# Kernel tuning notes

Measured on AMD Instinct MI355X. Metric: run time of the kernel, lower is better.

## Reference

```python
import jax, jax.numpy as jnp
import numpy as np

DIM = 256
FEATURE_SCALE = 4
NMS_THRESHOLD = 8.0
PRE_NMS_TOPK = 2048
MAX_OUTPUT = 256
MIN_SCORE = 0.2


def conv3d_same(x, w, b):
    # x: [D,H,W,Cin], w: [3,3,3,Cin,Cout] -> [D,H,W,Cout], SAME padding (flax default)
    y = jax.lax.conv_general_dilated(
        x[None], w, window_strides=(1, 1, 1), padding="SAME",
        dimension_numbers=("NDHWC", "DHWIO", "NDHWC"))
    return y[0] + b


def setup_inputs() -> dict:
    key = jax.random.key(0)
    ks = jax.random.split(key, 8)
    D, H, W, C = 16, 64, 64, 256
    feature = jax.random.normal(ks[0], (D, H, W, C), jnp.float32)
    mask = jax.random.bernoulli(ks[1], 0.8, (D * FEATURE_SCALE, H * FEATURE_SCALE, W * FEATURE_SCALE))
    s3a = 1.0 / np.sqrt(27 * C)
    s3b = 1.0 / np.sqrt(27 * DIM)
    s1 = 1.0 / np.sqrt(DIM)
    w0 = jax.random.normal(ks[2], (3, 3, 3, C, DIM), jnp.float32) * s3a
    b0 = jnp.zeros((DIM,), jnp.float32)
    w1 = jax.random.normal(ks[3], (3, 3, 3, DIM, DIM), jnp.float32) * s3b
    b1 = jnp.zeros((DIM,), jnp.float32)
    w_logit = jax.random.normal(ks[4], (DIM, 1), jnp.float32) * s1
    b_logit = jnp.zeros((1,), jnp.float32)
    w_reg = jax.random.normal(ks[5], (DIM, 3), jnp.float32) * s1
    b_reg = jnp.zeros((3,), jnp.float32)
    return dict(feature=feature, mask=mask, w0=w0, b0=b0, w1=w1, b1=b1,
                w_logit=w_logit, b_logit=b_logit, w_reg=w_reg, b_reg=b_reg)


def reference(feature, mask, w0, b0, w1, b1, w_logit, b_logit, w_reg, b_reg):
    # ---- feature mixing: n_layers=2 of conv3d + gelu (flax gelu is approximate/tanh) ----
    x = jax.nn.gelu(conv3d_same(feature, w0, b0))
    x = jax.nn.gelu(conv3d_same(x, w1, b1))
    D, H, W = x.shape[:3]

    # ---- detection block: 1x1 convs are pointwise dense layers ----
    logits = (x @ w_logit + b_logit)[..., 0].reshape(-1)          # [N]
    regressions = (x @ w_reg + b_reg)                              # [D,H,W,3]
    ref_locs = (jnp.moveaxis(jnp.mgrid[:D, :H, :W], 0, -1) + 0.5) * FEATURE_SCALE
    pred_locs = (ref_locs + regressions * FEATURE_SCALE).reshape(-1, 3)  # [N,3]

    # ---- generate_predictions: sigmoid scores, pre-NMS top-k, greedy distance NMS ----
    scores = jax.nn.sigmoid(logits)
    top_scores, idx = jax.lax.top_k(scores, PRE_NMS_TOPK)          # sorted desc
    top_locs = pred_locs[idx]                                      # [K,3]
    d2 = ((top_locs[:, None, :] - top_locs[None, :, :]) ** 2).sum(-1)  # [K,K]
    th2 = NMS_THRESHOLD * NMS_THRESHOLD

    def step(suppressed, i):
        keep_i = (~suppressed[i]) & (top_scores[i] >= MIN_SCORE)
        suppressed = suppressed | (keep_i & (d2[i] < th2))
        return suppressed, keep_i

    _, keep = jax.lax.scan(step, jnp.zeros((PRE_NMS_TOPK,), bool), jnp.arange(PRE_NMS_TOPK))
    sel_scores = jnp.where(keep, top_scores, 0.0)
    out_scores, oidx = jax.lax.top_k(sel_scores, MAX_OUTPUT)       # [M]
    out_locs = top_locs[oidx]                                      # [M,3]

    # ---- mask gather: floor/clip/index, zero out-of-mask scores ----
    pli = jnp.floor(out_locs).astype(jnp.int32)
    bound = jnp.array(mask.shape, jnp.int32) - 1
    plc = jnp.clip(pli, 0, bound)
    in_range = (pli == plc).all(axis=1)
    masked = jnp.where(in_range, mask[plc[:, 0], plc[:, 1], plc[:, 2]], False)
    out_scores = jnp.where(masked, out_scores, 0.0)

    return jnp.concatenate([out_locs, out_scores[:, None]], axis=-1)  # [M,4] = (z,y,x,score)
```

## Files before the change

kernel.cpp:

```cpp
#include <hip/hip_runtime.h>
#include <math.h>

#define Dz 16
#define Hy 64
#define Wx 64
#define CHN 256
#define NVOX (Dz*Hy*Wx)
#define TOPK 2048
#define MAXOUT 256
#define CAND_CAP 4096
#define NBCAP 16
#define NHIST 65536

typedef __attribute__((ext_vector_type(8))) _Float16 h8;
typedef __attribute__((ext_vector_type(8))) unsigned short u16x8;
typedef __attribute__((ext_vector_type(4))) float f32x4;

__device__ __forceinline__ float gelu_tanh(float x) {
    return 0.5f*x*(1.0f + tanhf(0.7978845608028654f*(x + 0.044715f*x*x*x)));
}
__device__ __forceinline__ unsigned f2sort(float f) {
    unsigned u = __float_as_uint(f);
    return (u & 0x80000000u) ? ~u : (u | 0x80000000u);
}
__device__ __forceinline__ float sort2f(unsigned s) {
    unsigned u = (s & 0x80000000u) ? (s & 0x7fffffffu) : ~s;
    return __uint_as_float(u);
}

#define MFMA(d, a, b) d = __builtin_amdgcn_mfma_f32_16x16x32_f16(a, b, d, 0, 0, 0)

__global__ __launch_bounds__(256) void prep_kernel(const float* __restrict__ w0,
        const float* __restrict__ w1, u16x8* __restrict__ wpk0,
        u16x8* __restrict__ wpk1, unsigned* __restrict__ hist,
        unsigned* __restrict__ counter) {
    int b = blockIdx.x, t = threadIdx.x;
    if (b < 1728) {
        int id = b*256 + t;
        int l = (id >= 221184) ? 1 : 0;
        int r = id - l*221184;
        int lane = r & 63, ng = (r >> 6) & 15, kbg = (r >> 10) & 7, tp = r >> 13;
        const float* w = l ? w1 : w0;
        u16x8* dst = l ? wpk1 : wpk0;
        h8 hv, lv;
        #pragma unroll
        for (int j = 0; j < 8; ++j) {
            int k = kbg*32 + (lane >> 4)*8 + j;
            int co = ng*16 + (lane & 15);
            float v = w[((size_t)tp*CHN + k)*CHN + co];
            _Float16 h = (_Float16)v;
            hv[j] = h;
            lv[j] = (_Float16)(v - (float)h);
        }
        size_t base = (((size_t)(tp*8 + kbg)*16 + ng)*2)*64 + lane;
        dst[base]      = __builtin_bit_cast(u16x8, hv);
        dst[base + 64] = __builtin_bit_cast(u16x8, lv);
    } else {
        int zb = b - 1728;
        int i = zb*256 + t;
        hist[i] = 0u; hist[i + 16384] = 0u; hist[i + 32768] = 0u; hist[i + 49152] = 0u;
        if (zb == 0 && t == 0) counter[0] = 0u;
    }
}

template<int LAYER>
__global__ __launch_bounds__(512, 4) void conv_kernel(
        const float* __restrict__ fsrc,
        const unsigned short* __restrict__ hhi, const unsigned short* __restrict__ hlo,
        const u16x8* __restrict__ wpk, const float* __restrict__ bias,
        unsigned short* __restrict__ ohi, unsigned short* __restrict__ olo,
        const float* __restrict__ wlog, const float* __restrict__ blog,
        const float* __restrict__ wreg, const float* __restrict__ breg,
        float* __restrict__ locs, unsigned long long* __restrict__ keys,
        unsigned* __restrict__ hist) {
    __shared__ h8 sm[4224];
    const int tid = threadIdx.x;
    const int lane = tid & 63, w = tid >> 6;
    const int yo = w >> 2, wn = w & 3;
    const int lr = lane & 15, lg = lane >> 4;
    const int z = blockIdx.y, y0 = blockIdx.x*2;

    f32x4 acc[4][4];
    #pragma unroll
    for (int m = 0; m < 4; ++m)
        #pragma unroll
        for (int n = 0; n < 4; ++n) acc[m][n] = (f32x4){0.f,0.f,0.f,0.f};

    for (int dz = 0; dz < 3; ++dz) {
        const int zz = z + dz - 1;
        for (int kc = 0; kc < 4; ++kc) {
            __syncthreads();
            if (LAYER == 0) {
                for (int cidx = tid; cidx < 2112; cidx += 512) {
                    int cd = cidx & 7;
                    int rr = cidx >> 3;
                    int r = rr % 66, iy = rr / 66;
                    int ygl = y0 - 1 + iy, xin = r - 1;
                    h8 hv = {0,0,0,0,0,0,0,0}, lv = {0,0,0,0,0,0,0,0};
                    if (((unsigned)zz < (unsigned)Dz) & ((unsigned)ygl < (unsigned)Hy)
                        & ((unsigned)xin < (unsigned)Wx)) {
                        const float* s = fsrc + ((size_t)((zz*Hy + ygl)*Wx + xin))*CHN
                                              + kc*64 + cd*8;
                        float4 t0 = *(const float4*)s;
                        float4 t1 = *(const float4*)(s + 4);
                        float vv[8] = {t0.x,t0.y,t0.z,t0.w,t1.x,t1.y,t1.z,t1.w};
                        #pragma unroll
                        for (int j = 0; j < 8; ++j) {
                            _Float16 h = (_Float16)vv[j];
                            hv[j] = h;
                            lv[j] = (_Float16)(vv[j] - (float)h);
                        }
                    }
                    int sl = cd ^ (r & 7);
                    sm[(iy*66 + r)*8 + sl] = hv;
                    sm[2112 + (iy*66 + r)*8 + sl] = lv;
                }
            } else {
                for (int cidx = tid; cidx < 4224; cidx += 512) {
                    int c = cidx & 7;
                    int rr = cidx >> 3;
                    int r = rr % 66, tt = rr / 66;
                    int p = tt >> 2, iy = tt & 3;
                    int ygl = y0 - 1 + iy, xin = r - 1;
                    u16x8 v = {0,0,0,0,0,0,0,0};
                    if (((unsigned)zz < (unsigned)Dz) & ((unsigned)ygl < (unsigned)Hy)
                        & ((unsigned)xin < (unsigned)Wx)) {
                        const unsigned short* bp = p ? hlo : hhi;
                        v = *(const u16x8*)(bp + ((size_t)((zz*Hy + ygl)*Wx + xin))*CHN
                                               + kc*64 + (size_t)((c ^ (r & 7)))*8);
                    }
                    sm[cidx] = __builtin_bit_cast(h8, v);
                }
            }
            __syncthreads();
            for (int dy = 0; dy < 3; ++dy) {
                const int iyA = yo + dy;
                const h8* As = sm + iyA*528;
                #pragma unroll
                for (int dx = 0; dx < 3; ++dx) {
                    const int tap = (dz*3 + dy)*3 + dx;
                    #pragma unroll
                    for (int kb = 0; kb < 2; ++kb) {
                        const int kbg = kc*2 + kb;
                        const u16x8* wb = wpk + ((size_t)(tap*8 + kbg)*32 + wn*8)*64 + lane;
                        h8 ah[4], al[4];
                        #pragma unroll
                        for (int m = 0; m < 4; ++m) {
                            const int r = m*16 + lr + dx;
                            const int sl = (kb*4 + lg) ^ (r & 7);
                            ah[m] = As[r*8 + sl];
                            al[m] = As[2112 + r*8 + sl];
                        }
                        #pragma unroll
                        for (int n = 0; n < 4; ++n) {
                            h8 bh = __builtin_bit_cast(h8, wb[(size_t)n*128]);
                            h8 bl = __builtin_bit_cast(h8, wb[(size_t)n*128 + 64]);
                            #pragma unroll
                            for (int m = 0; m < 4; ++m) MFMA(acc[m][n], ah[m], bh);
                            #pragma unroll
                            for (int m = 0; m < 4; ++m) MFMA(acc[m][n], al[m], bh);
                            #pragma unroll
                            for (int m = 0; m < 4; ++m) MFMA(acc[m][n], ah[m], bl);
                        }
                    }
                }
            }
        }
    }

    float bn[4];
    #pragma unroll
    for (int n = 0; n < 4; ++n) bn[n] = bias[wn*64 + n*16 + lr];

    if (LAYER == 0) {
        const int ygl = y0 + yo;
        #pragma unroll
        for (int m = 0; m < 4; ++m) {
            #pragma unroll
            for (int rg = 0; rg < 4; ++rg) {
                const int x = m*16 + lg*4 + rg;
                const size_t vbase = ((size_t)((z*Hy + ygl)*Wx + x))*CHN;
                #pragma unroll
                for (int n = 0; n < 4; ++n) {
                    const int co = wn*64 + n*16 + lr;
                    float g = gelu_tanh(acc[m][n][rg] + bn[n]);
                    _Float16 h = (_Float16)g;
                    _Float16 l = (_Float16)(g - (float)h);
                    ohi[vbase + co] = __builtin_bit_cast(unsigned short, h);
                    olo[vbase + co] = __builtin_bit_cast(unsigned short, l);
                }
            }
        }
    } else {
        float wl[4], wr0[4], wr1[4], wr2[4];
        #pragma unroll
        for (int n = 0; n < 4; ++n) {
            const int co = wn*64 + n*16 + lr;
            wl[n] = wlog[co];
            wr0[n] = wreg[co*3 + 0]; wr1[n] = wreg[co*3 + 1]; wr2[n] = wreg[co*3 + 2];
        }
        float p[4][16];
        #pragma unroll
        for (int c = 0; c < 4; ++c)
            #pragma unroll
            for (int xi = 0; xi < 16; ++xi) p[c][xi] = 0.f;
        #pragma unroll
        for (int m = 0; m < 4; ++m)
            #pragma unroll
            for (int rg = 0; rg < 4; ++rg) {
                const int xi = m*4 + rg;
                #pragma unroll
                for (int n = 0; n < 4; ++n) {
                    float g = gelu_tanh(acc[m][n][rg] + bn[n]);
                    p[0][xi] += g*wl[n];
                    p[1][xi] += g*wr0[n];
                    p[2][xi] += g*wr1[n];
                    p[3][xi] += g*wr2[n];
                }
            }
        #pragma unroll
        for (int st = 0; st < 4; ++st) {
            const int s = 1 << st;
            #pragma unroll
            for (int c = 0; c < 4; ++c)
                #pragma unroll
                for (int xi = 0; xi < 16; ++xi)
                    p[c][xi] += __shfl_xor(p[c][xi], s, 64);
        }
        __syncthreads();
        float* det = (float*)sm;
        if (lr == 0) {
            #pragma unroll
            for (int m = 0; m < 4; ++m)
                #pragma unroll
                for (int rg = 0; rg < 4; ++rg) {
                    const int x = m*16 + lg*4 + rg;
                    #pragma unroll
                    for (int c = 0; c < 4; ++c)
                        det[((yo*64 + x)*4 + c)*4 + wn] = p[c][m*4 + rg];
                }
        }
        __syncthreads();
        {
            const int yo2 = tid >> 8, x = (tid >> 2) & 63, chn = tid & 3;
            const float* dp = det + ((yo2*64 + x)*4 + chn)*4;
            float s = dp[0] + dp[1] + dp[2] + dp[3];
            const int ygl = y0 + yo2;
            const int vg = (z*Hy + ygl)*Wx + x;
            if (chn == 0) {
                float logit = s + blog[0];
                float score = 1.f/(1.f + expf(-logit));
                unsigned sb = f2sort(score);
                keys[vg] = ((unsigned long long)sb << 32)
                         | (unsigned long long)(0xFFFFFFFFu - (unsigned)vg);
                atomicAdd(&hist[sb >> 16], 1u);
            } else {
                float coord = (chn == 1) ? (float)z : (chn == 2) ? (float)ygl : (float)x;
                float loc = (coord + 0.5f)*4.0f + (s + breg[chn-1])*4.0f;
                locs[(size_t)vg*3 + (chn-1)] = loc;
            }
        }
    }
}

__global__ __launch_bounds__(1024) void find_cut_kernel(const unsigned* __restrict__ hist,
                                                        unsigned* __restrict__ cutp) {
    __shared__ unsigned ps[1024];
    __shared__ unsigned fs[64];
    __shared__ int sh_cb;
    __shared__ unsigned sh_acc;
    int t = threadIdx.x;
    unsigned s = 0;
    const unsigned* hp = hist + (size_t)t*64;
    for (int j = 0; j < 64; ++j) s += hp[j];
    ps[t] = s;
    __syncthreads();
    for (int off = 1; off < 1024; off <<= 1) {
        unsigned v = ps[t] + ((t + off < 1024) ? ps[t + off] : 0u);
        __syncthreads();
        ps[t] = v;
        __syncthreads();
    }
    if (ps[t] >= TOPK && (t == 1023 || ps[t+1] < TOPK)) {
        sh_cb = t; sh_acc = (t == 1023) ? 0u : ps[t+1];
    }
    __syncthreads();
    int cb = sh_cb; unsigned acc = sh_acc;
    if (t < 64) {
        unsigned f = acc;
        for (int u = t; u < 64; ++u) f += hist[(size_t)cb*64 + u];
        fs[t] = f;
    }
    __syncthreads();
    if (t < 64) {
        if (fs[t] >= TOPK && (t == 63 || fs[t+1] < TOPK))
            cutp[0] = ((unsigned)(cb*64 + t)) << 16;
    }
}

__global__ void compact_kernel(const unsigned long long* __restrict__ keys,
                               const unsigned* __restrict__ cutp,
                               unsigned* __restrict__ counter,
                               unsigned long long* __restrict__ cand) {
    int i = blockIdx.x*blockDim.x + threadIdx.x;
    unsigned thr = cutp[0];
    unsigned long long k = keys[i];
    if ((unsigned)(k >> 32) >= thr) {
        unsigned p = atomicAdd(counter, 1u);
        if (p < CAND_CAP) cand[p] = k;
    }
}

__global__ __launch_bounds__(128) void rank_kernel(const unsigned* __restrict__ counter,
        const unsigned long long* __restrict__ cand, const float* __restrict__ locs,
        float4* __restrict__ loc4G) {
    __shared__ unsigned long long kbuf[CAND_CAP];
    int t = threadIdx.x;
    int g = blockIdx.x*128 + t;
    int M = (int)*counter; if (M > CAND_CAP) M = CAND_CAP;
    for (int i = t; i < CAND_CAP; i += 128) kbuf[i] = (i < M) ? cand[i] : 0ull;
    __syncthreads();
    if (g >= M) return;
    unsigned long long mykey = kbuf[g];
    int rank = 0;
    for (int j = 0; j < M; ++j) rank += (kbuf[j] > mykey) ? 1 : 0;
    if (rank < TOPK) {
        unsigned idx = 0xFFFFFFFFu - (unsigned)(mykey & 0xFFFFFFFFull);
        float4 v;
        v.x = locs[(size_t)idx*3 + 0];
        v.y = locs[(size_t)idx*3 + 1];
        v.z = locs[(size_t)idx*3 + 2];
        v.w = sort2f((unsigned)(mykey >> 32));
        loc4G[rank] = v;
    }
}

__global__ __launch_bounds__(64) void nbr_kernel(const float4* __restrict__ loc4G,
        unsigned short* __restrict__ nbidx, unsigned char* __restrict__ nbcnt) {
    __shared__ float4 b4[TOPK];
    int t = threadIdx.x;
    int g = blockIdx.x*64 + t;
    for (int i = t; i < TOPK; i += 64) b4[i] = loc4G[i];
    __syncthreads();
    float4 me = b4[g];
    int cnt = 0;
    for (int j = 0; j < TOPK; ++j) {
        float4 o = b4[j];
        float dz = o.x - me.x, dy = o.y - me.y, dx = o.z - me.z;
        float d2 = dz*dz + dy*dy + dx*dx;
        if (d2 < 64.0f && j != g) {
            if (cnt < NBCAP) nbidx[(size_t)g*NBCAP + cnt] = (unsigned short)j;
            cnt++;
        }
    }
    nbcnt[g] = (unsigned char)min(cnt, 255);
}

__global__ __launch_bounds__(512) void nms_kernel(const float4* __restrict__ loc4G,
        const unsigned short* __restrict__ nbidx, const unsigned char* __restrict__ nbcnt,
        const int* __restrict__ mask, float* __restrict__ out) {
    __shared__ float4 p4[TOPK];
    __shared__ unsigned short snb[TOPK*NBCAP];
    __shared__ unsigned char scnt[TOPK];
    __shared__ unsigned char supf[TOPK];
    __shared__ unsigned char keepB[TOPK];
    __shared__ unsigned keepw[64];
    __shared__ int wpre[64];
    __shared__ int sh_nk;
    int t = threadIdx.x;
    for (int i = t; i < TOPK; i += 512) {
        p4[i] = loc4G[i]; scnt[i] = nbcnt[i]; supf[i] = 0; keepB[i] = 0;
    }
    for (int i = t; i < TOPK*NBCAP/8; i += 512)
        ((uint4*)snb)[i] = ((const uint4*)nbidx)[i];
    __syncthreads();
    if (t < 64) {
        const int l = t;
        float cz[32], cy[32], cx[32];
        #pragma unroll
        for (int j = 0; j < 32; ++j) {
            float4 v = p4[l*32 + j];
            cz[j] = v.x; cy[j] = v.y; cx[j] = v.z;
        }
        int myok = 0;
        #pragma unroll
        for (int j = 0; j < 32; ++j) myok += (p4[l*32 + j].w >= 0.2f) ? 1 : 0;
        #pragma unroll
        for (int s = 1; s < 64; s <<= 1) myok += __shfl_xor(myok, s, 64);
        const int NS = myok;
        int keeps = 0;
        for (int i = 0; i < NS; ++i) {
            bool kept = (supf[i] == 0);
            if (kept) {
                if (l == 0) keepB[i] = 1;
                ++keeps;
                const int cnt = scnt[i];
                if (cnt <= NBCAP) {
                    if (l < cnt) supf[snb[i*NBCAP + l]] = 1;
                } else {
                    float4 pv = p4[i];
                    #pragma unroll
                    for (int j = 0; j < 32; ++j) {
                        float dz = cz[j]-pv.x, dy = cy[j]-pv.y, dx = cx[j]-pv.z;
                        if (dz*dz + dy*dy + dx*dx < 64.0f) supf[l*32 + j] = 1;
                    }
                }
                asm volatile("s_waitcnt lgkmcnt(0)" ::: "memory");
                if (keeps >= MAXOUT) break;
            }
        }
    }
    __syncthreads();
    if (t < 64) {
        unsigned wmask = 0u;
        for (int j = 0; j < 32; ++j) wmask |= (keepB[t*32 + j] ? 1u : 0u) << j;
        keepw[t] = wmask;
    }
    __syncthreads();
    if (t < 64) {
        int p = 0;
        for (int j = 0; j < t; ++j) p += __popc(keepw[j]);
        wpre[t] = p;
        if (t == 63) sh_nk = p + __popc(keepw[63]);
    }
    __syncthreads();
    const int nk = sh_nk;
    for (int i = t; i < TOPK; i += 512) {
        unsigned w = keepw[i >> 5];
        bool kp = (w >> (i & 31)) & 1u;
        int rk = wpre[i >> 5] + __popc(w & ((1u << (i & 31)) - 1u));
        int slot = kp ? rk : (nk + (i - rk));
        if (slot < MAXOUT) {
            float4 v = p4[i];
            float lz = v.x, ly = v.y, lx = v.z;
            float sc = kp ? v.w : 0.f;
            int iz = (int)floorf(lz), iy = (int)floorf(ly), ix = (int)floorf(lx);
            int cz2 = min(max(iz,0),Dz*4-1), cy2 = min(max(iy,0),Hy*4-1), cx2 = min(max(ix,0),Wx*4-1);
            bool inr = (iz==cz2) && (iy==cy2) && (ix==cx2);
            float osc = (inr && mask[((size_t)cz2*(Hy*4) + cy2)*(Wx*4) + cx2] != 0) ? sc : 0.f;
            out[slot*4+0] = lz; out[slot*4+1] = ly; out[slot*4+2] = lx; out[slot*4+3] = osc;
        }
    }
}

extern "C" void kernel_launch(void* const* d_in, const int* in_sizes, int n_in,
                              void* d_out, int out_size, void* d_ws, size_t ws_size,
                              hipStream_t stream) {
    const float* feature = (const float*)d_in[0];
    const int*   mask    = (const int*)d_in[1];
    const float* w0   = (const float*)d_in[2];
    const float* b0   = (const float*)d_in[3];
    const float* w1   = (const float*)d_in[4];
    const float* b1   = (const float*)d_in[5];
    const float* wlog = (const float*)d_in[6];
    const float* blog = (const float*)d_in[7];
    const float* wreg = (const float*)d_in[8];
    const float* breg = (const float*)d_in[9];

    char* ws = (char*)d_ws;
    size_t off = 0;
    unsigned short* h1hi = (unsigned short*)(ws + off); off += (size_t)NVOX*CHN*2;
    unsigned short* h1lo = (unsigned short*)(ws + off); off += (size_t)NVOX*CHN*2;
    u16x8* wpk0 = (u16x8*)(ws + off);               off += (size_t)442368*16;
    u16x8* wpk1 = (u16x8*)(ws + off);               off += (size_t)442368*16;
    unsigned long long* keys = (unsigned long long*)(ws + off); off += (size_t)NVOX*8;
    float* locs = (float*)(ws + off);               off += (size_t)NVOX*3*4;
    unsigned* hist = (unsigned*)(ws + off);         off += (size_t)NHIST*4;
    unsigned* counter = (unsigned*)(ws + off);      off += 256;
    unsigned* cutp = counter + 1;
    unsigned long long* cand = (unsigned long long*)(ws + off); off += (size_t)CAND_CAP*8;
    float4* loc4G = (float4*)(ws + off);            off += (size_t)TOPK*16;
    unsigned short* nbidx = (unsigned short*)(ws + off); off += (size_t)TOPK*NBCAP*2;
    unsigned char* nbcnt = (unsigned char*)(ws + off);   off += (size_t)TOPK;
    if (ws_size < off) return;

    prep_kernel<<<1792, 256, 0, stream>>>(w0, w1, wpk0, wpk1, hist, counter);
    dim3 cgrid(Hy/2, Dz);
    conv_kernel<0><<<cgrid, 512, 0, stream>>>(feature, nullptr, nullptr, wpk0, b0,
                                              h1hi, h1lo,
                                              nullptr, nullptr, nullptr, nullptr,
                                              nullptr, nullptr, nullptr);
    conv_kernel<1><<<cgrid, 512, 0, stream>>>(nullptr, h1hi, h1lo, wpk1, b1,
                                              nullptr, nullptr,
                                              wlog, blog, wreg, breg,
                                              locs, keys, hist);
    find_cut_kernel<<<1, 1024, 0, stream>>>(hist, cutp);
    compact_kernel<<<NVOX/256, 256, 0, stream>>>(keys, cutp, counter, cand);
    rank_kernel<<<CAND_CAP/128, 128, 0, stream>>>(counter, cand, locs, loc4G);
    nbr_kernel<<<TOPK/64, 64, 0, stream>>>(loc4G, nbidx, nbcnt);
    nms_kernel<<<1, 512, 0, stream>>>(loc4G, nbidx, nbcnt, mask, (float*)d_out);
}
```

Measured before the change: 1.592 ms.

## Re-tile conv waves to 8x2 MFMA tiles and swizzle block order

Changes each wave's tile in the conv kernels from 4 rows x 64 output channels (one y row) to 8 rows x 32 channels (both y rows), so each wave loads half as many weight fragments from global memory but reads more LDS A fragments. The A fragments are now loaded inside the MFMA loop rather than held in arrays, which may lower register pressure. The grid becomes 1D with a swizzled block-to-(z,y) mapping, likely to improve L2 locality of weight and input reads across concurrently running blocks. The detection-head reduction is restructured to reduce per m-tile and sum 8 wave partials through LDS.

```diff
diff --git a/kernel.cpp b/kernel.cpp
--- a/kernel.cpp
+++ b/kernel.cpp
@@ -75,16 +75,17 @@
         unsigned* __restrict__ hist) {
     __shared__ h8 sm[4224];
     const int tid = threadIdx.x;
-    const int lane = tid & 63, w = tid >> 6;
-    const int yo = w >> 2, wn = w & 3;
+    const int lane = tid & 63, wn = tid >> 6;
     const int lr = lane & 15, lg = lane >> 4;
-    const int z = blockIdx.y, y0 = blockIdx.x*2;
-
-    f32x4 acc[4][4];
+    const int bid = blockIdx.x;
+    const int swz = (bid & 7)*64 + (bid >> 3);
+    const int z = swz >> 5, y0 = (swz & 31)*2;
+
+    f32x4 acc[8][2];
     #pragma unroll
-    for (int m = 0; m < 4; ++m)
-        #pragma unroll
-        for (int n = 0; n < 4; ++n) acc[m][n] = (f32x4){0.f,0.f,0.f,0.f};
+    for (int m = 0; m < 8; ++m)
+        #pragma unroll
+        for (int n = 0; n < 2; ++n) acc[m][n] = (f32x4){0.f,0.f,0.f,0.f};
 
     for (int dz = 0; dz < 3; ++dz) {
         const int zz = z + dz - 1;
@@ -134,33 +135,38 @@
             }
             __syncthreads();
             for (int dy = 0; dy < 3; ++dy) {
-                const int iyA = yo + dy;
-                const h8* As = sm + iyA*528;
                 #pragma unroll
                 for (int dx = 0; dx < 3; ++dx) {
                     const int tap = (dz*3 + dy)*3 + dx;
                     #pragma unroll
                     for (int kb = 0; kb < 2; ++kb) {
                         const int kbg = kc*2 + kb;
-                        const u16x8* wb = wpk + ((size_t)(tap*8 + kbg)*32 + wn*8)*64 + lane;
-                        h8 ah[4], al[4];
+                        const u16x8* wb = wpk + ((size_t)(tap*8 + kbg)*32 + wn*4)*64 + lane;
+                        h8 bh0 = __builtin_bit_cast(h8, wb[0]);
+                        h8 bh1 = __builtin_bit_cast(h8, wb[128]);
                         #pragma unroll
-                        for (int m = 0; m < 4; ++m) {
-                            const int r = m*16 + lr + dx;
+                        for (int m = 0; m < 8; ++m) {
+                            const int iyA = (m >> 2) + dy;
+                            const int r = (m & 3)*16 + lr + dx;
                             const int sl = (kb*4 + lg) ^ (r & 7);
-                            ah[m] = As[r*8 + sl];
-                            al[m] = As[2112 + r*8 + sl];
+                            const int base = (iyA*66 + r)*8 + sl;
+                            h8 ah = sm[base];
+                            h8 al = sm[2112 + base];
+                            MFMA(acc[m][0], ah, bh0);
+                            MFMA(acc[m][0], al, bh0);
+                            MFMA(acc[m][1], ah, bh1);
+                            MFMA(acc[m][1], al, bh1);
                         }
+                        h8 bl0 = __builtin_bit_cast(h8, wb[64]);
+                        h8 bl1 = __builtin_bit_cast(h8, wb[192]);
                         #pragma unroll
-                        for (int n = 0; n < 4; ++n) {
-                            h8 bh = __builtin_bit_cast(h8, wb[(size_t)n*128]);
-                            h8 bl = __builtin_bit_cast(h8, wb[(size_t)n*128 + 64]);
-                            #pragma unroll
-                            for (int m = 0; m < 4; ++m) MFMA(acc[m][n], ah[m], bh);
-                            #pragma unroll
-                            for (int m = 0; m < 4; ++m) MFMA(acc[m][n], al[m], bh);
-                            #pragma unroll
-                            for (int m = 0; m < 4; ++m) MFMA(acc[m][n], ah[m], bl);
+                        for (int m = 0; m < 8; ++m) {
+                            const int iyA = (m >> 2) + dy;
+                            const int r = (m & 3)*16 + lr + dx;
+                            const int sl = (kb*4 + lg) ^ (r & 7);
+                            h8 ah = sm[(iyA*66 + r)*8 + sl];
+                            MFMA(acc[m][0], ah, bl0);
+                            MFMA(acc[m][1], ah, bl1);
                         }
                     }
                 }
@@ -168,21 +174,21 @@
         }
     }
 
-    float bn[4];
+    float bn[2];
     #pragma unroll
-    for (int n = 0; n < 4; ++n) bn[n] = bias[wn*64 + n*16 + lr];
+    for (int n = 0; n < 2; ++n) bn[n] = bias[wn*32 + n*16 + lr];
 
     if (LAYER == 0) {
-        const int ygl = y0 + yo;
-        #pragma unroll
-        for (int m = 0; m < 4; ++m) {
+        #pragma unroll
+        for (int m = 0; m < 8; ++m) {
+            const int ygl = y0 + (m >> 2);
             #pragma unroll
             for (int rg = 0; rg < 4; ++rg) {
-                const int x = m*16 + lg*4 + rg;
+                const int x = (m & 3)*16 + lg*4 + rg;
                 const size_t vbase = ((size_t)((z*Hy + ygl)*Wx + x))*CHN;
                 #pragma unroll
-                for (int n = 0; n < 4; ++n) {
-                    const int co = wn*64 + n*16 + lr;
+                for (int n = 0; n < 2; ++n) {
+                    const int co = wn*32 + n*16 + lr;
                     float g = gelu_tanh(acc[m][n][rg] + bn[n]);
                     _Float16 h = (_Float16)g;
                     _Float16 l = (_Float16)(g - (float)h);
@@ -192,60 +198,58 @@
             }
         }
     } else {
-        float wl[4], wr0[4], wr1[4], wr2[4];
-        #pragma unroll
-        for (int n = 0; n < 4; ++n) {
-            const int co = wn*64 + n*16 + lr;
+        float wl[2], wr0[2], wr1[2], wr2[2];
+        #pragma unroll
+        for (int n = 0; n < 2; ++n) {
+            const int co = wn*32 + n*16 + lr;
             wl[n] = wlog[co];
             wr0[n] = wreg[co*3 + 0]; wr1[n] = wreg[co*3 + 1]; wr2[n] = wreg[co*3 + 2];
         }
-        float p[4][16];
-        #pragma unroll
-        for (int c = 0; c < 4; ++c)
-            #pragma unroll
-            for (int xi = 0; xi < 16; ++xi) p[c][xi] = 0.f;
-        #pragma unroll
-        for (int m = 0; m < 4; ++m)
-            #pragma unroll
-            for (int rg = 0; rg < 4; ++rg) {
-                const int xi = m*4 + rg;
-                #pragma unroll
-                for (int n = 0; n < 4; ++n) {
-                    float g = gelu_tanh(acc[m][n][rg] + bn[n]);
-                    p[0][xi] += g*wl[n];
-                    p[1][xi] += g*wr0[n];
-                    p[2][xi] += g*wr1[n];
-                    p[3][xi] += g*wr2[n];
-                }
-            }
-        #pragma unroll
-        for (int st = 0; st < 4; ++st) {
-            const int s = 1 << st;
+        __syncthreads();
+        float* det = (float*)sm;
+        #pragma unroll
+        for (int m = 0; m < 8; ++m) {
+            float p[4][4];
             #pragma unroll
             for (int c = 0; c < 4; ++c)
                 #pragma unroll
-                for (int xi = 0; xi < 16; ++xi)
-                    p[c][xi] += __shfl_xor(p[c][xi], s, 64);
-        }
-        __syncthreads();
-        float* det = (float*)sm;
-        if (lr == 0) {
+                for (int rg = 0; rg < 4; ++rg) p[c][rg] = 0.f;
             #pragma unroll
-            for (int m = 0; m < 4; ++m)
+            for (int rg = 0; rg < 4; ++rg)
+                #pragma unroll
+                for (int n = 0; n < 2; ++n) {
+                    float g = gelu_tanh(acc[m][n][rg] + bn[n]);
+                    p[0][rg] += g*wl[n];
+                    p[1][rg] += g*wr0[n];
+                    p[2][rg] += g*wr1[n];
+                    p[3][rg] += g*wr2[n];
+                }
+            #pragma unroll
+            for (int st = 0; st < 4; ++st) {
+                const int s = 1 << st;
+                #pragma unroll
+                for (int c = 0; c < 4; ++c)
+                    #pragma unroll
+                    for (int rg = 0; rg < 4; ++rg)
+                        p[c][rg] += __shfl_xor(p[c][rg], s, 64);
+            }
+            if (lr == 0) {
+                const int yrow = m >> 2;
                 #pragma unroll
                 for (int rg = 0; rg < 4; ++rg) {
-                    const int x = m*16 + lg*4 + rg;
+                    const int x = (m & 3)*16 + lg*4 + rg;
                     #pragma unroll
                     for (int c = 0; c < 4; ++c)
-                        det[((yo*64 + x)*4 + c)*4 + wn] = p[c][m*4 + rg];
-                }
+                        det[((yrow*64 + x)*4 + c)*8 + wn] = p[c][rg];
+                }
+            }
         }
         __syncthreads();
         {
-            const int yo2 = tid >> 8, x = (tid >> 2) & 63, chn = tid & 3;
-            const float* dp = det + ((yo2*64 + x)*4 + chn)*4;
-            float s = dp[0] + dp[1] + dp[2] + dp[3];
-            const int ygl = y0 + yo2;
+            const int vox = tid >> 2, chn = tid & 3;
+            const float* dp = det + ((size_t)(vox*4 + chn))*8;
+            float s = dp[0] + dp[1] + dp[2] + dp[3] + dp[4] + dp[5] + dp[6] + dp[7];
+            const int ygl = y0 + (vox >> 6), x = vox & 63;
             const int vg = (z*Hy + ygl)*Wx + x;
             if (chn == 0) {
                 float logit = s + blog[0];
@@ -475,15 +479,14 @@
     if (ws_size < off) return;
 
     prep_kernel<<<1792, 256, 0, stream>>>(w0, w1, wpk0, wpk1, hist, counter);
-    dim3 cgrid(Hy/2, Dz);
-    conv_kernel<0><<<cgrid, 512, 0, stream>>>(feature, nullptr, nullptr, wpk0, b0,
-                                              h1hi, h1lo,
-                                              nullptr, nullptr, nullptr, nullptr,
-                                              nullptr, nullptr, nullptr);
-    conv_kernel<1><<<cgrid, 512, 0, stream>>>(nullptr, h1hi, h1lo, wpk1, b1,
-                                              nullptr, nullptr,
-                                              wlog, blog, wreg, breg,
-                                              locs, keys, hist);
+    conv_kernel<0><<<512, 512, 0, stream>>>(feature, nullptr, nullptr, wpk0, b0,
+                                            h1hi, h1lo,
+                                            nullptr, nullptr, nullptr, nullptr,
+                                            nullptr, nullptr, nullptr);
+    conv_kernel<1><<<512, 512, 0, stream>>>(nullptr, h1hi, h1lo, wpk1, b1,
+                                            nullptr, nullptr,
+                                            wlog, blog, wreg, breg,
+                                            locs, keys, hist);
     find_cut_kernel<<<1, 1024, 0, stream>>>(hist, cutp);
     compact_kernel<<<NVOX/256, 256, 0, stream>>>(keys, cutp, counter, cand);
     rank_kernel<<<CAND_CAP/128, 128, 0, stream>>>(counter, cand, locs, loc4G);
```

Result: faster. 1.506 ms (-5.4%).
